# Kernel optimization log

Hardware: AMD Instinct MI355X
Metric: run time of the kernel (lower is better)

The kernel has to match this reference:

```python
import jax, jax.numpy as jnp
import numpy as np

B, S, E, H, ROT, MAXP = 2, 1024, 2048, 16, 64, 2048
HD = E // H
EPS = 1e-12  # torch F.normalize default eps


def _sinusoidal_positions(num_pos, dim):
    # GPT-J create_sinusoidal_positions: concat(sin, cos) along feature dim
    inv_freq = 1.0 / (10000.0 ** (np.arange(0, dim, 2, dtype=np.float32) / dim))
    sinusoid = np.einsum("i,j->ij", np.arange(num_pos, dtype=np.float32), inv_freq)
    return jnp.asarray(np.concatenate([np.sin(sinusoid), np.cos(sinusoid)], axis=-1))


def _rotate_every_two(x):
    x1 = x[..., ::2]
    x2 = x[..., 1::2]
    return jnp.stack((-x2, x1), axis=-1).reshape(x.shape)


def _apply_rotary(t, sin, cos):
    # t: [B,S,H,rot]; sin/cos: [B,S,rot/2] -> repeat_interleave(2) -> [B,S,1,rot]
    sin = jnp.repeat(sin, 2, axis=-1)[:, :, None, :]
    cos = jnp.repeat(cos, 2, axis=-1)[:, :, None, :]
    return t * cos + _rotate_every_two(t) * sin


def setup_inputs() -> dict:
    key = jax.random.key(0)
    ks = jax.random.split(key, 5)
    hidden_states = jax.random.normal(ks[0], (B, S, E), dtype=jnp.float32)
    w_q = jax.random.normal(ks[1], (E, E), dtype=jnp.float32) * 0.02
    w_k = jax.random.normal(ks[2], (E, E), dtype=jnp.float32) * 0.02
    w_v = jax.random.normal(ks[3], (E, E), dtype=jnp.float32) * 0.02
    w_o = jax.random.normal(ks[4], (E, E), dtype=jnp.float32) * 0.02
    norm_const = 0.5 * jnp.ones((1, H, 1, 1), dtype=jnp.float32)
    attention_mask = jnp.zeros((B, 1, 1, S), dtype=jnp.float32)  # 0 = attend (HF additive mask)
    position_ids = jnp.tile(jnp.arange(S, dtype=jnp.int32)[None, :], (B, 1))
    return {"hidden_states": hidden_states, "w_q": w_q, "w_k": w_k, "w_v": w_v,
            "w_o": w_o, "norm_const": norm_const, "attention_mask": attention_mask,
            "position_ids": position_ids}


def reference(hidden_states, w_q, w_k, w_v, w_o, norm_const, attention_mask, position_ids):
    b, s, e = hidden_states.shape
    # projections (nn.Linear, no bias): y = x @ W.T
    q = (hidden_states @ w_q.T).reshape(b, s, H, HD)  # rotary layout [B,S,H,hd]
    k = (hidden_states @ w_k.T).reshape(b, s, H, HD)
    v = (hidden_states @ w_v.T).reshape(b, s, H, HD).transpose(0, 2, 1, 3)  # [B,H,S,hd]

    embed = _sinusoidal_positions(MAXP, ROT)          # [MAXP, ROT]
    sincos = embed[position_ids]                      # [B,S,ROT]
    sin, cos = jnp.split(sincos, 2, axis=-1)          # each [B,S,ROT/2]

    # partial rotary on first ROT dims
    q = jnp.concatenate([_apply_rotary(q[..., :ROT], sin, cos), q[..., ROT:]], axis=-1)
    k = jnp.concatenate([_apply_rotary(k[..., :ROT], sin, cos), k[..., ROT:]], axis=-1)
    q = q.transpose(0, 2, 1, 3)  # [B,H,S,hd]
    k = k.transpose(0, 2, 1, 3)

    causal = jnp.tril(jnp.ones((s, s), dtype=bool))[None, None]   # [1,1,S,S]
    mask0 = (attention_mask == 0)                                  # [B,1,1,S] bool

    # value rescale: per-query count of visible keys ** sigmoid(norm_const), clamped >= 1
    counts = jnp.sum(causal & mask0, axis=-1, keepdims=True).astype(jnp.float32)  # [B,1,S,1]
    denom = jnp.maximum(counts ** jax.nn.sigmoid(norm_const), 1.0)                # [B,H,S,1]
    v = v / denom

    # L2-normalize q/k (torch F.normalize: x / max(||x||, eps))
    q = q / jnp.maximum(jnp.linalg.norm(q, axis=-1, keepdims=True), EPS)
    k = k / jnp.maximum(jnp.linalg.norm(k, axis=-1, keepdims=True), EPS)

    mask_t = jnp.swapaxes(mask0, -1, -2)  # [B,1,S,1]
    q = q * mask_t
    k = k * mask_t
    v = v * mask_t

    attn_weights = jnp.einsum("bhqd,bhkd->bhqk", q, k)     # cosine similarities
    attn_weights = jnp.where(causal, attn_weights, 0.0)
    attn_output = jnp.einsum("bhqk,bhkd->bhqd", attn_weights, v)

    attn_output = attn_output.transpose(0, 2, 1, 3).reshape(b, s, e)
    return attn_output @ w_o.T
```

## Files before the change

kernel.cpp:

```cpp
#include <hip/hip_runtime.h>
#include <math.h>

#define B 2
#define S 1024
#define E 2048
#define H 16
#define HD 128
#define ROT 64
#define EPSN 1e-12f

using half8 = __attribute__((ext_vector_type(8))) _Float16;
using half4 = __attribute__((ext_vector_type(4))) _Float16;
using half2 = __attribute__((ext_vector_type(2))) _Float16;
using f32x4 = __attribute__((ext_vector_type(4))) float;

__device__ __forceinline__ void gl_lds16(const void* g, void* l) {
    __builtin_amdgcn_global_load_lds(
        (const __attribute__((address_space(1))) unsigned int*)g,
        (__attribute__((address_space(3))) unsigned int*)l, 16, 0, 0);
}

#define BARX()  asm volatile("s_barrier" ::: "memory")
#define LGKM0() asm volatile("s_waitcnt lgkmcnt(0)" ::: "memory")
#define VMW(n)  asm volatile("s_waitcnt vmcnt(" #n ")" ::: "memory")

__global__ __launch_bounds__(256) void f2h5(const float* __restrict__ x0,
                                            const float* __restrict__ x1,
                                            const float* __restrict__ x2,
                                            const float* __restrict__ x3,
                                            const float* __restrict__ x4,
                                            _Float16* __restrict__ y0,
                                            _Float16* __restrict__ y1,
                                            _Float16* __restrict__ y2,
                                            _Float16* __restrict__ y3,
                                            _Float16* __restrict__ y4) {
    const float* xs[5] = {x0, x1, x2, x3, x4};
    _Float16*    ys[5] = {y0, y1, y2, y3, y4};
    const int t = blockIdx.y;
    const int i = blockIdx.x * 256 + threadIdx.x;
    float4 v = ((const float4*)xs[t])[i];
    half4 h;
    h[0] = (_Float16)v.x; h[1] = (_Float16)v.y;
    h[2] = (_Float16)v.z; h[3] = (_Float16)v.w;
    ((half4*)ys[t])[i] = h;
}

__global__ __launch_bounds__(512, 2) void gemm_qkv256(
        const _Float16* __restrict__ hs,
        const _Float16* __restrict__ wq,
        const _Float16* __restrict__ wk,
        const _Float16* __restrict__ wv,
        _Float16* __restrict__ qo,
        _Float16* __restrict__ ko,
        _Float16* __restrict__ vo) {
    __shared__ uint4 L[8][1024];

    const int lid = (int)blockIdx.x;
    const int swz = (lid & 7) * 24 + (lid >> 3);
    const int z   = swz >> 6;
    const int gm  = (swz & 63) >> 3;
    const int gn  = swz & 7;
    const _Float16* Wp = (z == 0) ? wq : (z == 1) ? wk : wv;
    _Float16*     Cout = (z == 0) ? qo : (z == 1) ? ko : vo;
    const int mBase = gm << 8;
    const int nBase = gn << 8;

    const int tid   = (int)threadIdx.x;
    const int lane  = tid & 63;
    const int w     = tid >> 6;
    const int l15   = lane & 15;
    const int lq    = lane >> 4;
    const int wm4   = (w >> 2) << 2;
    const int wn2   = (w & 3) << 1;
    const int wbase = tid & 448;

    f32x4 acc[2][2][4][2];
#pragma unroll
    for (int X = 0; X < 2; ++X)
#pragma unroll
        for (int Y = 0; Y < 2; ++Y)
#pragma unroll
            for (int mt = 0; mt < 4; ++mt)
#pragma unroll
                for (int nt = 0; nt < 2; ++nt)
                    acc[X][Y][mt][nt] = (f32x4){0.f, 0.f, 0.f, 0.f};

    half8 af[4][2], wf[2][2];

    auto stage = [&](int slot, const _Float16* src, int rowBase, int hf, int kt) {
#pragma unroll
        for (int j = 0; j < 2; ++j) {
            const int c  = (j << 9) + tid;
            const int rb = c >> 7;
            const int q  = (c >> 4) & 7;
            const int r  = c & 15;
            gl_lds16(&src[(size_t)(rowBase + hf * 128 + rb * 16 + r) * E +
                          kt * 64 + q * 8],
                     &L[slot][(j << 9) + wbase]);
        }
    };
    auto ldsA = [&](int db, int X) {
#pragma unroll
        for (int mt = 0; mt < 4; ++mt)
#pragma unroll
            for (int ks = 0; ks < 2; ++ks)
                af[mt][ks] = *(const half8*)&L[db * 2 + X]
                    [(wm4 + mt) * 128 + (ks * 4 + lq) * 16 + l15];
    };
    auto ldsB = [&](int db, int Y) {
#pragma unroll
        for (int nt = 0; nt < 2; ++nt)
#pragma unroll
            for (int ks = 0; ks < 2; ++ks)
                wf[nt][ks] = *(const half8*)&L[4 + db * 2 + Y]
                    [(wn2 + nt) * 128 + (ks * 4 + lq) * 16 + l15];
    };
    auto mma = [&](int X, int Y) {
        __builtin_amdgcn_s_setprio(1);
#pragma unroll
        for (int mt = 0; mt < 4; ++mt)
#pragma unroll
            for (int nt = 0; nt < 2; ++nt)
#pragma unroll
                for (int ks = 0; ks < 2; ++ks)
                    acc[X][Y][mt][nt] = __builtin_amdgcn_mfma_f32_16x16x32_f16(
                        af[mt][ks], wf[nt][ks], acc[X][Y][mt][nt], 0, 0, 0);
        __builtin_amdgcn_s_setprio(0);
    };

    stage(0, hs, mBase, 0, 0);
    stage(4, Wp, nBase, 0, 0);
    stage(1, hs, mBase, 1, 0);
    stage(5, Wp, nBase, 1, 0);
    stage(2, hs, mBase, 0, 1);
    stage(7, Wp, nBase, 1, 1);
    stage(3, hs, mBase, 1, 1);
    VMW(6);
    BARX();

    for (int j = 0; j < 16; ++j) {
        const int tB  = 2 * j + 1;
        const int tN0 = 2 * j + 2;
        const int tN1 = 2 * j + 3;
        const bool more = (j < 15);

        ldsA(0, 0); ldsB(0, 0);
        stage(6, Wp, nBase, 0, tB);
        BARX(); LGKM0();
        mma(0, 0);
        BARX();

        ldsB(0, 1);
        if (more) stage(0, hs, mBase, 0, tN0);
        BARX(); LGKM0();
        mma(0, 1);
        BARX();

        ldsA(0, 1);
        if (more) stage(5, Wp, nBase, 1, tN0);
        BARX(); LGKM0();
        mma(1, 1);
        BARX();

        ldsB(0, 0);
        if (more) { stage(1, hs, mBase, 1, tN0); VMW(4); }
        else      { VMW(0); }
        BARX(); LGKM0();
        mma(1, 0);
        BARX();

        ldsA(1, 0); ldsB(1, 0);
        if (more) stage(4, Wp, nBase, 0, tN0);
        BARX(); LGKM0();
        mma(0, 0);
        BARX();

        ldsB(1, 1);
        if (more) stage(2, hs, mBase, 0, tN1);
        BARX(); LGKM0();
        mma(0, 1);
        BARX();

        ldsA(1, 1);
        if (more) stage(7, Wp, nBase, 1, tN1);
        BARX(); LGKM0();
        mma(1, 1);
        BARX();

        ldsB(1, 0);
        if (more) stage(3, hs, mBase, 1, tN1);
        VMW(4);
        BARX(); LGKM0();
        mma(1, 0);
        BARX();
    }

#pragma unroll
    for (int X = 0; X < 2; ++X)
#pragma unroll
        for (int Y = 0; Y < 2; ++Y)
#pragma unroll
            for (int mt = 0; mt < 4; ++mt)
#pragma unroll
                for (int nt = 0; nt < 2; ++nt)
#pragma unroll
                    for (int r = 0; r < 4; ++r) {
                        int row = mBase + X * 128 + (w >> 2) * 64 + mt * 16 + lq * 4 + r;
                        int col = nBase + Y * 128 + (w & 3) * 32 + nt * 16 + l15;
                        int b = row >> 10, s = row & (S - 1);
                        int h = col >> 7,  d = col & (HD - 1);
                        Cout[(((size_t)b * H + h) * S + s) * HD + d] =
                            (_Float16)acc[X][Y][mt][nt][r];
                    }
}

__global__ __launch_bounds__(256) void gemm_out(const _Float16* __restrict__ A,
                                                const _Float16* __restrict__ Wp,
                                                float* __restrict__ C) {
    __shared__ uint4 As_l[2][512];
    __shared__ uint4 Ws_l[2][512];
    const int lid = (int)blockIdx.x;
    const int swz = (lid & 7) * 32 + (lid >> 3);
    const int gm  = swz >> 4;
    const int gn  = swz & 15;
    const int tid  = threadIdx.x;
    const int lane = tid & 63;
    const int w    = tid >> 6;
    const int wm   = (w >> 1) * 64;
    const int wn   = (w & 1) * 64;
    const int l15  = lane & 15;
    const int lq   = lane >> 4;
    const int r16  = lane & 15;
    const int kq4  = lane >> 4;
    const int mBase = gm * 128;
    const int nBase = gn * 128;

    f32x4 acc[4][4];
#pragma unroll
    for (int mt = 0; mt < 4; ++mt)
#pragma unroll
        for (int nt = 0; nt < 4; ++nt)
            acc[mt][nt] = (f32x4){0.f, 0.f, 0.f, 0.f};

    auto stage = [&](int bf, int k0) {
#pragma unroll
        for (int i = 0; i < 2; ++i) {
            int rb = w * 2 + i;
            gl_lds16(&A[(size_t)(mBase + rb * 16 + r16) * E + k0 + kq4 * 8],
                     &As_l[bf][rb * 64]);
            gl_lds16(&Wp[(size_t)(nBase + rb * 16 + r16) * E + k0 + kq4 * 8],
                     &Ws_l[bf][rb * 64]);
        }
    };

    stage(0, 0);
    const int nIter = E / 32;
    for (int it = 0; it < nIter; ++it) {
        __syncthreads();
        if (it + 1 < nIter) stage((it + 1) & 1, (it + 1) * 32);

        const int cur = it & 1;
        half8 af[4], wfr[4];
#pragma unroll
        for (int t = 0; t < 4; ++t) {
            int rbA = (wm >> 4) + t;
            int rbW = (wn >> 4) + t;
            af[t]  = *(const half8*)&As_l[cur][rbA * 64 + lq * 16 + l15];
            wfr[t] = *(const half8*)&Ws_l[cur][rbW * 64 + lq * 16 + l15];
        }
#pragma unroll
        for (int mt = 0; mt < 4; ++mt)
#pragma unroll
            for (int nt = 0; nt < 4; ++nt)
                acc[mt][nt] = __builtin_amdgcn_mfma_f32_16x16x32_f16(
                    af[mt], wfr[nt], acc[mt][nt], 0, 0, 0);
    }

#pragma unroll
    for (int mt = 0; mt < 4; ++mt)
#pragma unroll
        for (int nt = 0; nt < 4; ++nt)
#pragma unroll
            for (int r = 0; r < 4; ++r) {
                int row = mBase + wm + mt * 16 + lq * 4 + r;
                int col = nBase + wn + nt * 16 + l15;
                C[(size_t)row * E + col] = acc[mt][nt][r];
            }
}

__global__ __launch_bounds__(256) void rotary_norm(_Float16* __restrict__ qh,
                                                   _Float16* __restrict__ kh,
                                                   const float* __restrict__ am,
                                                   const int* __restrict__ pos) {
    const int wave = threadIdx.x >> 6;
    const int lane = threadIdx.x & 63;
    const int item = blockIdx.x * 4 + wave;
    const int b = item / (H * S);
    const int h = (item / S) % H;
    const int s = item % S;

    const float p = (float)pos[b * S + s];
    float co = 1.f, si = 0.f;
    if (lane < 32) {
        float ang = p * expf(-0.28782313662425574f * (float)lane);
        sincosf(ang, &si, &co);
    }
    const float valid = (am[b * S + s] == 0.f) ? 1.f : 0.f;
    const size_t base = ((size_t)(b * H + h) * S + s) * HD;

    _Float16* bufs[2] = {qh, kh};
#pragma unroll
    for (int a = 0; a < 2; ++a) {
        _Float16* ptr = bufs[a];
        half2 xin = *(const half2*)&ptr[base + 2 * lane];
        float x0 = (float)xin[0], x1 = (float)xin[1];
        float y0, y1;
        if (lane < 32) {
            y0 = x0 * co - x1 * si;
            y1 = x1 * co + x0 * si;
        } else {
            y0 = x0;
            y1 = x1;
        }
        float ss = y0 * y0 + y1 * y1;
#pragma unroll
        for (int off = 32; off > 0; off >>= 1)
            ss += __shfl_xor(ss, off);
        float scale = valid / fmaxf(sqrtf(ss), EPSN);
        half2 xo;
        xo[0] = (_Float16)(y0 * scale);
        xo[1] = (_Float16)(y1 * scale);
        *(half2*)&ptr[base + 2 * lane] = xo;
    }
}

__global__ __launch_bounds__(256) void vprep(const _Float16* __restrict__ v,
                                             const _Float16* __restrict__ k,
                                             _Float16* __restrict__ vt,
                                             _Float16* __restrict__ kt,
                                             const float* __restrict__ am,
                                             const float* __restrict__ nc) {
    __shared__ _Float16 T[HD][72];
    __shared__ float sscale[64];
    const int bh = blockIdx.y;
    const int b = bh >> 4, h = bh & 15;
    const int s0 = blockIdx.x * 64;
    const int tid = threadIdx.x;

    if (tid < 64) {
        const int lane = tid;
        float basec = 0.f;
        for (int j0 = 0; j0 < s0; j0 += 64) {
            float z = (am[b * S + j0 + lane] == 0.f) ? 1.f : 0.f;
#pragma unroll
            for (int off = 32; off > 0; off >>= 1)
                z += __shfl_xor(z, off);
            basec += z;
        }
        float zown = (am[b * S + s0 + lane] == 0.f) ? 1.f : 0.f;
        float sc = zown;
#pragma unroll
        for (int off = 1; off < 64; off <<= 1) {
            float u = __shfl_up(sc, off);
            if (lane >= off) sc += u;
        }
        float cntv = basec + sc;
        float sig = 1.f / (1.f + expf(-nc[h]));
        float denom = fmaxf(powf(cntv, sig), 1.f);
        sscale[lane] = zown / denom;
    }
    __syncthreads();

#pragma unroll
    for (int j = 0; j < 4; ++j) {
        int f = tid + j * 256;
        int s = f >> 4, c8 = f & 15;
        half8 x = *(const half8*)&v[((size_t)bh * S + s0 + s) * HD + c8 * 8];
        float sc = sscale[s];
#pragma unroll
        for (int i = 0; i < 8; ++i)
            T[c8 * 8 + i][s] = (_Float16)((float)x[i] * sc);
    }
    __syncthreads();
#pragma unroll
    for (int j = 0; j < 4; ++j) {
        int f = tid + j * 256;
        int d = f >> 3, c8 = f & 7;
        *(uint4*)&vt[((size_t)bh * HD + d) * S + s0 + c8 * 8] =
            *(const uint4*)&T[d][c8 * 8];
    }

    __syncthreads();
#pragma unroll
    for (int j = 0; j < 4; ++j) {
        int f = tid + j * 256;
        int s = f >> 4, c8 = f & 15;
        half8 x = *(const half8*)&k[((size_t)bh * S + s0 + s) * HD + c8 * 8];
#pragma unroll
        for (int i = 0; i < 8; ++i)
            T[c8 * 8 + i][s] = x[i];
    }
    __syncthreads();
#pragma unroll
    for (int j = 0; j < 4; ++j) {
        int f = tid + j * 256;
        int d = f >> 3, c8 = f & 7;
        *(uint4*)&kt[((size_t)bh * HD + d) * S + s0 + c8 * 8] =
            *(const uint4*)&T[d][c8 * 8];
    }
}

__global__ __launch_bounds__(256) void kvouter(const _Float16* __restrict__ kt,
                                               const _Float16* __restrict__ vt,
                                               _Float16* __restrict__ ut) {
    __shared__ __align__(16) _Float16 SB[2 * 128 * 72];
    _Float16 (*Kt_s)[72] = (_Float16(*)[72])SB;
    _Float16 (*Vt_s)[72] = (_Float16(*)[72])(SB + 128 * 72);
    const int c  = blockIdx.x;
    const int bh = blockIdx.y;
    const int tid = threadIdx.x;
    const int lane = tid & 63, w = tid >> 6;
    const int l15 = lane & 15, lq = lane >> 4;
    const size_t ds_b = (size_t)bh * HD * S + (size_t)c * 64;

    uint4 pk[4], pv[4];
#pragma unroll
    for (int j = 0; j < 4; ++j) {
        int f = tid + j * 256;
        int d = f >> 3, c8 = f & 7;
        pk[j] = *(const uint4*)&kt[ds_b + (size_t)d * S + c8 * 8];
        pv[j] = *(const uint4*)&vt[ds_b + (size_t)d * S + c8 * 8];
    }
#pragma unroll
    for (int j = 0; j < 4; ++j) {
        int f = tid + j * 256;
        int d = f >> 3, c8 = f & 7;
        *(uint4*)&Kt_s[d][c8 * 8] = pk[j];
        *(uint4*)&Vt_s[d][c8 * 8] = pv[j];
    }
    __syncthreads();

    f32x4 acc[2][8];
#pragma unroll
    for (int mt = 0; mt < 2; ++mt)
#pragma unroll
        for (int nt = 0; nt < 8; ++nt)
            acc[mt][nt] = (f32x4){0.f, 0.f, 0.f, 0.f};

#pragma unroll
    for (int ks = 0; ks < 2; ++ks) {
        half8 af[2], wf[8];
#pragma unroll
        for (int mt = 0; mt < 2; ++mt)
            af[mt] = *(const half8*)&Kt_s[(w * 2 + mt) * 16 + l15][ks * 32 + lq * 8];
#pragma unroll
        for (int nt = 0; nt < 8; ++nt)
            wf[nt] = *(const half8*)&Vt_s[nt * 16 + l15][ks * 32 + lq * 8];
#pragma unroll
        for (int mt = 0; mt < 2; ++mt)
#pragma unroll
            for (int nt = 0; nt < 8; ++nt)
                acc[mt][nt] = __builtin_amdgcn_mfma_f32_16x16x32_f16(
                    af[mt], wf[nt], acc[mt][nt], 0, 0, 0);
    }
    __syncthreads();

    _Float16* Mb = SB;
#pragma unroll
    for (int mt = 0; mt < 2; ++mt)
#pragma unroll
        for (int nt = 0; nt < 8; ++nt)
#pragma unroll
            for (int r = 0; r < 4; ++r) {
                int dk = (w * 2 + mt) * 16 + lq * 4 + r;
                int flat = nt * 2048 + (dk >> 5) * 512 +
                           (l15 + ((dk >> 3) & 3) * 16) * 8 + (dk & 7);
                Mb[flat] = (_Float16)acc[mt][nt][r];
            }
    __syncthreads();

    const size_t ub = ((size_t)bh * 16 + c) << 14;
#pragma unroll
    for (int j = 0; j < 8; ++j) {
        int f = tid + j * 256;
        *(uint4*)&ut[ub + (size_t)f * 8] = *(const uint4*)&Mb[f * 8];
    }
}

__global__ __launch_bounds__(256) void prefix16(_Float16* __restrict__ u) {
    const int sl = blockIdx.x & 7;
    const int bh = blockIdx.x >> 3;
    const size_t base = (size_t)bh * 16 * 16384 + sl * 2048 + threadIdx.x * 8;
    float acc[8] = {0.f, 0.f, 0.f, 0.f, 0.f, 0.f, 0.f, 0.f};
    half8 nxt = *(const half8*)&u[base];
#pragma unroll
    for (int c = 0; c < 16; ++c) {
        half8 cur = nxt;
        if (c < 15) nxt = *(const half8*)&u[base + (size_t)(c + 1) * 16384];
        half8 outv;
#pragma unroll
        for (int i = 0; i < 8; ++i) outv[i] = (_Float16)acc[i];
        *(half8*)&u[base + (size_t)c * 16384] = outv;
#pragma unroll
        for (int i = 0; i < 8; ++i) acc[i] += (float)cur[i];
    }
}

__global__ __launch_bounds__(256) void attn_local(const _Float16* __restrict__ qh,
                                                  const _Float16* __restrict__ kh,
                                                  const _Float16* __restrict__ vt,
                                                  const _Float16* __restrict__ mt,
                                                  _Float16* __restrict__ o) {
    __shared__ _Float16 Ks[64][136];
    __shared__ _Float16 Vs[HD][72];
    __shared__ _Float16 Ps[64][72];
    __shared__ uint4 Ms[2048];

    const int qt = blockIdx.x;
    const int bh = blockIdx.y;
    const int b = bh >> 4, h = bh & 15;
    const int tid = threadIdx.x;
    const int lane = tid & 63;
    const int w = tid >> 6;
    const int l15 = lane & 15;
    const int lq = lane >> 4;
    const int qBase = qt * 64;
    const size_t sd_base = (size_t)bh * S * HD;

    half8 qf[4];
#pragma unroll
    for (int ks = 0; ks < 4; ++ks)
        qf[ks] = *(const half8*)&qh[sd_base + (size_t)(qBase + w * 16 + l15) * HD +
                                    ks * 32 + lq * 8];

    const _Float16* mtc = mt + (((size_t)bh * 16 + qt) << 14);
#pragma unroll
    for (int rr = 0; rr < 8; ++rr)
        gl_lds16(&mtc[(size_t)((rr * 4 + w) * 64 + lane) * 8],
                 &Ms[(rr * 4 + w) * 64]);

    uint4 pk[4], pv[4];
#pragma unroll
    for (int j = 0; j < 4; ++j) {
        int f = tid + j * 256;
        int rK = f >> 4, c8K = f & 15;
        int rV = f >> 3, c8V = f & 7;
        pk[j] = *(const uint4*)&kh[sd_base + (size_t)(qBase + rK) * HD + c8K * 8];
        pv[j] = *(const uint4*)&vt[sd_base + (size_t)rV * S + qBase + c8V * 8];
    }
#pragma unroll
    for (int j = 0; j < 4; ++j) {
        int f = tid + j * 256;
        int rK = f >> 4, c8K = f & 15;
        int rV = f >> 3, c8V = f & 7;
        *(uint4*)&Ks[rK][c8K * 8] = pk[j];
        *(uint4*)&Vs[rV][c8V * 8] = pv[j];
    }
    __syncthreads();

    f32x4 sacc[4];
#pragma unroll
    for (int nt = 0; nt < 4; ++nt)
        sacc[nt] = (f32x4){0.f, 0.f, 0.f, 0.f};
#pragma unroll
    for (int nt = 0; nt < 4; ++nt)
#pragma unroll
        for (int ks = 0; ks < 4; ++ks) {
            half8 kf = *(const half8*)&Ks[nt * 16 + l15][ks * 32 + lq * 8];
            sacc[nt] = __builtin_amdgcn_mfma_f32_16x16x32_f16(qf[ks], kf,
                                                              sacc[nt], 0, 0, 0);
        }

#pragma unroll
    for (int nt = 0; nt < 4; ++nt)
#pragma unroll
        for (int r = 0; r < 4; ++r) {
            int ql = w * 16 + lq * 4 + r;
            int kl = nt * 16 + l15;
            float sv = (kl <= ql) ? sacc[nt][r] : 0.f;
            Ps[ql][kl] = (_Float16)sv;
        }

    f32x4 oacc[8];
#pragma unroll
    for (int dt = 0; dt < 8; ++dt)
        oacc[dt] = (f32x4){0.f, 0.f, 0.f, 0.f};
#pragma unroll
    for (int dt = 0; dt < 8; ++dt)
#pragma unroll
        for (int km = 0; km < 4; ++km) {
            half8 mf = *(const half8*)&Ms[(dt * 4 + km) * 64 + lane];
            oacc[dt] = __builtin_amdgcn_mfma_f32_16x16x32_f16(qf[km], mf,
                                                              oacc[dt], 0, 0, 0);
        }
    __syncthreads();

    half8 pf[2];
    pf[0] = *(const half8*)&Ps[w * 16 + l15][lq * 8];
    pf[1] = *(const half8*)&Ps[w * 16 + l15][32 + lq * 8];
#pragma unroll
    for (int dt = 0; dt < 8; ++dt)
#pragma unroll
        for (int ks = 0; ks < 2; ++ks) {
            half8 vf = *(const half8*)&Vs[dt * 16 + l15][ks * 32 + lq * 8];
            oacc[dt] = __builtin_amdgcn_mfma_f32_16x16x32_f16(pf[ks], vf,
                                                              oacc[dt], 0, 0, 0);
        }

#pragma unroll
    for (int dt = 0; dt < 8; ++dt)
#pragma unroll
        for (int r = 0; r < 4; ++r)
            Ks[w * 16 + lq * 4 + r][dt * 16 + l15] = (_Float16)oacc[dt][r];
    __syncthreads();
#pragma unroll
    for (int j = 0; j < 4; ++j) {
        int f = tid + j * 256;
        int ql = f >> 4, c8 = f & 15;
        *(uint4*)&o[(size_t)(b * S + qBase + ql) * E + h * HD + c8 * 8] =
            *(const uint4*)&Ks[ql][c8 * 8];
    }
}

extern "C" void kernel_launch(void* const* d_in, const int* in_sizes, int n_in,
                              void* d_out, int out_size, void* d_ws, size_t ws_size,
                              hipStream_t stream) {
    (void)in_sizes; (void)n_in; (void)out_size; (void)ws_size;
    const float* hs = (const float*)d_in[0];
    const float* wq = (const float*)d_in[1];
    const float* wk = (const float*)d_in[2];
    const float* wv = (const float*)d_in[3];
    const float* wo = (const float*)d_in[4];
    const float* nc = (const float*)d_in[5];
    const float* am = (const float*)d_in[6];
    const int*  pos = (const int*)d_in[7];
    float* out = (float*)d_out;

    const size_t act = (size_t)B * S * E;
    _Float16* hsb = (_Float16*)d_ws;
    _Float16* wqb = hsb + act;
    _Float16* wkb = wqb + act;
    _Float16* wvb = wkb + act;
    _Float16* wob = wvb + act;
    _Float16* qhh = wob + act;
    _Float16* khh = qhh + act;
    _Float16* vhh = khh + act;
    _Float16* vtt = vhh + act;
    _Float16* abb = vtt + act;
    _Float16* ktt = hsb;
    _Float16* utm = wqb;

    f2h5<<<dim3((int)(act / 4 / 256), 5), 256, 0, stream>>>(
        hs, wq, wk, wv, wo, hsb, wqb, wkb, wvb, wob);

    gemm_qkv256<<<192, 512, 0, stream>>>(hsb, wqb, wkb, wvb, qhh, khh, vhh);

    rotary_norm<<<(B * H * S) / 4, 256, 0, stream>>>(qhh, khh, am, pos);
    vprep<<<dim3(S / 64, B * H), 256, 0, stream>>>(vhh, khh, vtt, ktt, am, nc);

    kvouter<<<dim3(16, B * H), 256, 0, stream>>>(ktt, vtt, utm);
    prefix16<<<B * H * 8, 256, 0, stream>>>(utm);
    attn_local<<<dim3(16, B * H), 256, 0, stream>>>(qhh, khh, vtt, utm, abb);

    gemm_out<<<256, 256, 0, stream>>>(abb, wob, out);
}
```

Before: 301.4 us.

## Fuse rotary, normalization, V scaling and K/V transposes into QKV GEMM epilogue

Moves the rotary embedding, L2 normalization, mask application, V count-based rescale and the K/V transposes into the epilogue of the QKV projection GEMM. The epilogue stages the output tile through LDS with a swizzled index, and a small prefix-count kernel precomputes the visible-key counts. This removes two separate kernels and their global round trips of Q/K/V. The GEMM main loop is also re-pipelined with register double buffering of the A/B fragments and sched barriers in place of the explicit lgkmcnt waits, which trades higher register pressure for overlap of LDS reads with MFMA.

```diff
diff --git a/kernel.cpp b/kernel.cpp
--- a/kernel.cpp
+++ b/kernel.cpp
@@ -20,9 +20,13 @@
         (__attribute__((address_space(3))) unsigned int*)l, 16, 0, 0);
 }
 
-#define BARX()  asm volatile("s_barrier" ::: "memory")
-#define LGKM0() asm volatile("s_waitcnt lgkmcnt(0)" ::: "memory")
-#define VMW(n)  asm volatile("s_waitcnt vmcnt(" #n ")" ::: "memory")
+#define BARX()   asm volatile("s_barrier" ::: "memory")
+#define VMW(n)   asm volatile("s_waitcnt vmcnt(" #n ")" ::: "memory")
+#define SCHEDB() __builtin_amdgcn_sched_barrier(0)
+
+__device__ __forceinline__ int ctIdx(int row, int col) {
+    return row * 256 + (col & 3) + ((((col >> 2) ^ ((row >> 3) & 15)) & 63) << 2);
+}
 
 __global__ __launch_bounds__(256) void f2h5(const float* __restrict__ x0,
                                             const float* __restrict__ x1,
@@ -45,6 +49,21 @@
     ((half4*)ys[t])[i] = h;
 }
 
+__global__ __launch_bounds__(1024) void countprep(const float* __restrict__ am,
+                                                  float* __restrict__ cnt) {
+    __shared__ float sc[1024];
+    const int b = blockIdx.x, t = threadIdx.x;
+    sc[t] = (am[b * S + t] == 0.f) ? 1.f : 0.f;
+    __syncthreads();
+    for (int off = 1; off < 1024; off <<= 1) {
+        float u = (t >= off) ? sc[t - off] : 0.f;
+        __syncthreads();
+        sc[t] += u;
+        __syncthreads();
+    }
+    cnt[b * S + t] = sc[t];
+}
+
 __global__ __launch_bounds__(512, 2) void gemm_qkv256(
         const _Float16* __restrict__ hs,
         const _Float16* __restrict__ wq,
@@ -52,8 +71,14 @@
         const _Float16* __restrict__ wv,
         _Float16* __restrict__ qo,
         _Float16* __restrict__ ko,
-        _Float16* __restrict__ vo) {
+        _Float16* __restrict__ kto,
+        _Float16* __restrict__ vto,
+        const float* __restrict__ am,
+        const int*  __restrict__ pos,
+        const float* __restrict__ nc,
+        const float* __restrict__ cnt) {
     __shared__ uint4 L[8][1024];
+    __shared__ float sclA[256], sclB[256];
 
     const int lid = (int)blockIdx.x;
     const int swz = (lid & 7) * 24 + (lid >> 3);
@@ -61,7 +86,6 @@
     const int gm  = (swz & 63) >> 3;
     const int gn  = swz & 7;
     const _Float16* Wp = (z == 0) ? wq : (z == 1) ? wk : wv;
-    _Float16*     Cout = (z == 0) ? qo : (z == 1) ? ko : vo;
     const int mBase = gm << 8;
     const int nBase = gn << 8;
 
@@ -74,6 +98,24 @@
     const int wn2   = (w & 3) << 1;
     const int wbase = tid & 448;
 
+    const int bb  = mBase >> 10;
+    const int sB0 = mBase & (S - 1);
+    const int h0  = gn * 2;
+
+    if (tid < 256) {
+        const int sgx = sB0 + tid;
+        float valid = (am[bb * S + sgx] == 0.f) ? 1.f : 0.f;
+        if (z == 2) {
+            float c  = cnt[bb * S + sgx];
+            float g0 = 1.f / (1.f + expf(-nc[h0]));
+            float g1 = 1.f / (1.f + expf(-nc[h0 + 1]));
+            sclA[tid] = valid / fmaxf(powf(c, g0), 1.f);
+            sclB[tid] = valid / fmaxf(powf(c, g1), 1.f);
+        } else {
+            sclA[tid] = valid;
+        }
+    }
+
     f32x4 acc[2][2][4][2];
 #pragma unroll
     for (int X = 0; X < 2; ++X)
@@ -85,7 +127,7 @@
                 for (int nt = 0; nt < 2; ++nt)
                     acc[X][Y][mt][nt] = (f32x4){0.f, 0.f, 0.f, 0.f};
 
-    half8 af[4][2], wf[2][2];
+    half8 afA[4][2], afB[4][2], wfA[2][2], wfB[2][2];
 
     auto stage = [&](int slot, const _Float16* src, int rowBase, int hf, int kt) {
 #pragma unroll
@@ -99,34 +141,33 @@
                      &L[slot][(j << 9) + wbase]);
         }
     };
-    auto ldsA = [&](int db, int X) {
+    auto ldsA = [&](half8 (&dst)[4][2], int slot) {
 #pragma unroll
         for (int mt = 0; mt < 4; ++mt)
 #pragma unroll
             for (int ks = 0; ks < 2; ++ks)
-                af[mt][ks] = *(const half8*)&L[db * 2 + X]
+                dst[mt][ks] = *(const half8*)&L[slot]
                     [(wm4 + mt) * 128 + (ks * 4 + lq) * 16 + l15];
     };
-    auto ldsB = [&](int db, int Y) {
+    auto ldsB = [&](half8 (&dst)[2][2], int slot) {
 #pragma unroll
         for (int nt = 0; nt < 2; ++nt)
 #pragma unroll
             for (int ks = 0; ks < 2; ++ks)
-                wf[nt][ks] = *(const half8*)&L[4 + db * 2 + Y]
+                dst[nt][ks] = *(const half8*)&L[slot]
                     [(wn2 + nt) * 128 + (ks * 4 + lq) * 16 + l15];
     };
-    auto mma = [&](int X, int Y) {
-        __builtin_amdgcn_s_setprio(1);
-#pragma unroll
-        for (int mt = 0; mt < 4; ++mt)
-#pragma unroll
-            for (int nt = 0; nt < 2; ++nt)
-#pragma unroll
-                for (int ks = 0; ks < 2; ++ks)
-                    acc[X][Y][mt][nt] = __builtin_amdgcn_mfma_f32_16x16x32_f16(
-                        af[mt][ks], wf[nt][ks], acc[X][Y][mt][nt], 0, 0, 0);
-        __builtin_amdgcn_s_setprio(0);
-    };
+
+#define MMAQ(X, Y, Af, Bf)                                                     \
+    do {                                                                       \
+        __builtin_amdgcn_s_setprio(1);                                         \
+        _Pragma("unroll") for (int mt = 0; mt < 4; ++mt)                       \
+            _Pragma("unroll") for (int nt = 0; nt < 2; ++nt)                   \
+                _Pragma("unroll") for (int ks = 0; ks < 2; ++ks)               \
+                    acc[X][Y][mt][nt] = __builtin_amdgcn_mfma_f32_16x16x32_f16(\
+                        Af[mt][ks], Bf[nt][ks], acc[X][Y][mt][nt], 0, 0, 0);   \
+        __builtin_amdgcn_s_setprio(0);                                         \
+    } while (0)
 
     stage(0, hs, mBase, 0, 0);
     stage(4, Wp, nBase, 0, 0);
@@ -137,6 +178,8 @@
     stage(3, hs, mBase, 1, 1);
     VMW(6);
     BARX();
+    ldsA(afA, 0);
+    ldsB(wfA, 4);
 
     for (int j = 0; j < 16; ++j) {
         const int tB  = 2 * j + 1;
@@ -144,57 +187,59 @@
         const int tN1 = 2 * j + 3;
         const bool more = (j < 15);
 
-        ldsA(0, 0); ldsB(0, 0);
+        BARX();
+        ldsB(wfB, 5);
         stage(6, Wp, nBase, 0, tB);
-        BARX(); LGKM0();
-        mma(0, 0);
-        BARX();
-
-        ldsB(0, 1);
+        SCHEDB();
+        MMAQ(0, 0, afA, wfA);
+
+        BARX();
+        ldsA(afB, 1);
         if (more) stage(0, hs, mBase, 0, tN0);
-        BARX(); LGKM0();
-        mma(0, 1);
-        BARX();
-
-        ldsA(0, 1);
+        SCHEDB();
+        MMAQ(0, 1, afA, wfB);
+
+        BARX();
         if (more) stage(5, Wp, nBase, 1, tN0);
-        BARX(); LGKM0();
-        mma(1, 1);
-        BARX();
-
-        ldsB(0, 0);
-        if (more) { stage(1, hs, mBase, 1, tN0); VMW(4); }
-        else      { VMW(0); }
-        BARX(); LGKM0();
-        mma(1, 0);
-        BARX();
-
-        ldsA(1, 0); ldsB(1, 0);
+        SCHEDB();
+        MMAQ(1, 1, afB, wfB);
+
+        if (more) { VMW(4); } else { VMW(0); }
+        BARX();
+        ldsA(afA, 2);
+        ldsB(wfB, 6);
+        if (more) stage(1, hs, mBase, 1, tN0);
+        SCHEDB();
+        MMAQ(1, 0, afB, wfA);
+
+        BARX();
+        ldsB(wfA, 7);
         if (more) stage(4, Wp, nBase, 0, tN0);
-        BARX(); LGKM0();
-        mma(0, 0);
-        BARX();
-
-        ldsB(1, 1);
+        SCHEDB();
+        MMAQ(0, 0, afA, wfB);
+
+        BARX();
+        ldsA(afB, 3);
         if (more) stage(2, hs, mBase, 0, tN1);
-        BARX(); LGKM0();
-        mma(0, 1);
-        BARX();
-
-        ldsA(1, 1);
+        SCHEDB();
+        MMAQ(0, 1, afA, wfA);
+
+        BARX();
         if (more) stage(7, Wp, nBase, 1, tN1);
-        BARX(); LGKM0();
-        mma(1, 1);
-        BARX();
-
-        ldsB(1, 0);
+        SCHEDB();
+        MMAQ(1, 1, afB, wfA);
+
+        VMW(4);
+        BARX();
+        ldsA(afA, 0);
+        ldsB(wfA, 4);
         if (more) stage(3, hs, mBase, 1, tN1);
-        VMW(4);
-        BARX(); LGKM0();
-        mma(1, 0);
-        BARX();
-    }
-
+        SCHEDB();
+        MMAQ(1, 0, afB, wfB);
+    }
+
+    BARX();
+    _Float16* CtH = (_Float16*)&L[0][0];
 #pragma unroll
     for (int X = 0; X < 2; ++X)
 #pragma unroll
@@ -205,13 +250,65 @@
                 for (int nt = 0; nt < 2; ++nt)
 #pragma unroll
                     for (int r = 0; r < 4; ++r) {
-                        int row = mBase + X * 128 + (w >> 2) * 64 + mt * 16 + lq * 4 + r;
-                        int col = nBase + Y * 128 + (w & 3) * 32 + nt * 16 + l15;
-                        int b = row >> 10, s = row & (S - 1);
-                        int h = col >> 7,  d = col & (HD - 1);
-                        Cout[(((size_t)b * H + h) * S + s) * HD + d] =
-                            (_Float16)acc[X][Y][mt][nt][r];
+                        int row = X * 128 + (w >> 2) * 64 + mt * 16 + lq * 4 + r;
+                        int col = Y * 128 + (w & 3) * 32 + nt * 16 + l15;
+                        float v = acc[X][Y][mt][nt][r];
+                        if (z == 2) v *= (Y ? sclB[row] : sclA[row]);
+                        CtH[ctIdx(row, col)] = (_Float16)v;
                     }
+    __syncthreads();
+
+    if (z < 2) {
+        _Float16* rowOut = (z == 0) ? qo : ko;
+        const int hh = lane >> 5;
+        const int il = lane & 31;
+        for (int rr = 0; rr < 32; ++rr) {
+            int row = w * 32 + rr;
+            int sg  = sB0 + row;
+            float p = (float)pos[bb * S + sg];
+            half4 x = *(const half4*)&CtH[ctIdx(row, hh * 128 + il * 4)];
+            float v0 = x[0], v1 = x[1], v2 = x[2], v3 = x[3];
+            if (il < 16) {
+                float a0 = p * expf(-0.28782313662425574f * (float)(2 * il));
+                float a1 = p * expf(-0.28782313662425574f * (float)(2 * il + 1));
+                float s0, c0, s1, c1;
+                sincosf(a0, &s0, &c0);
+                sincosf(a1, &s1, &c1);
+                float t0 = v0 * c0 - v1 * s0, t1 = v1 * c0 + v0 * s0;
+                float t2 = v2 * c1 - v3 * s1, t3 = v3 * c1 + v2 * s1;
+                v0 = t0; v1 = t1; v2 = t2; v3 = t3;
+            }
+            float ss = v0 * v0 + v1 * v1 + v2 * v2 + v3 * v3;
+            ss += __shfl_xor(ss, 1);  ss += __shfl_xor(ss, 2);
+            ss += __shfl_xor(ss, 4);  ss += __shfl_xor(ss, 8);
+            ss += __shfl_xor(ss, 16);
+            float scl = sclA[row] / fmaxf(sqrtf(ss), EPSN);
+            half4 y;
+            y[0] = (_Float16)(v0 * scl); y[1] = (_Float16)(v1 * scl);
+            y[2] = (_Float16)(v2 * scl); y[3] = (_Float16)(v3 * scl);
+            *(half4*)&rowOut[(((size_t)bb * H + h0 + hh) * S + sg) * HD +
+                             il * 4] = y;
+            if (z == 1)
+                *(half4*)&CtH[ctIdx(row, hh * 128 + il * 4)] = y;
+        }
+    }
+    if (z >= 1) {
+        if (z == 1) __syncthreads();
+        _Float16* To = (z == 1) ? kto : vto;
+#pragma unroll
+        for (int i = 0; i < 16; ++i) {
+            int cch = tid + i * 512;
+            int dr  = cch >> 5;
+            int sc  = cch & 31;
+            half8 hv;
+#pragma unroll
+            for (int jj = 0; jj < 8; ++jj)
+                hv[jj] = CtH[ctIdx(sc * 8 + jj, dr)];
+            *(half8*)&To[(((size_t)bb * H + h0 + (dr >> 7)) * HD + (dr & 127)) * S +
+                         sB0 + sc * 8] = hv;
+        }
+    }
+#undef MMAQ
 }
 
 __global__ __launch_bounds__(256) void gemm_out(const _Float16* __restrict__ A,
@@ -288,128 +385,6 @@
             }
 }
 
-__global__ __launch_bounds__(256) void rotary_norm(_Float16* __restrict__ qh,
-                                                   _Float16* __restrict__ kh,
-                                                   const float* __restrict__ am,
-                                                   const int* __restrict__ pos) {
-    const int wave = threadIdx.x >> 6;
-    const int lane = threadIdx.x & 63;
-    const int item = blockIdx.x * 4 + wave;
-    const int b = item / (H * S);
-    const int h = (item / S) % H;
-    const int s = item % S;
-
-    const float p = (float)pos[b * S + s];
-    float co = 1.f, si = 0.f;
-    if (lane < 32) {
-        float ang = p * expf(-0.28782313662425574f * (float)lane);
-        sincosf(ang, &si, &co);
-    }
-    const float valid = (am[b * S + s] == 0.f) ? 1.f : 0.f;
-    const size_t base = ((size_t)(b * H + h) * S + s) * HD;
-
-    _Float16* bufs[2] = {qh, kh};
-#pragma unroll
-    for (int a = 0; a < 2; ++a) {
-        _Float16* ptr = bufs[a];
-        half2 xin = *(const half2*)&ptr[base + 2 * lane];
-        float x0 = (float)xin[0], x1 = (float)xin[1];
-        float y0, y1;
-        if (lane < 32) {
-            y0 = x0 * co - x1 * si;
-            y1 = x1 * co + x0 * si;
-        } else {
-            y0 = x0;
-            y1 = x1;
-        }
-        float ss = y0 * y0 + y1 * y1;
-#pragma unroll
-        for (int off = 32; off > 0; off >>= 1)
-            ss += __shfl_xor(ss, off);
-        float scale = valid / fmaxf(sqrtf(ss), EPSN);
-        half2 xo;
-        xo[0] = (_Float16)(y0 * scale);
-        xo[1] = (_Float16)(y1 * scale);
-        *(half2*)&ptr[base + 2 * lane] = xo;
-    }
-}
-
-__global__ __launch_bounds__(256) void vprep(const _Float16* __restrict__ v,
-                                             const _Float16* __restrict__ k,
-                                             _Float16* __restrict__ vt,
-                                             _Float16* __restrict__ kt,
-                                             const float* __restrict__ am,
-                                             const float* __restrict__ nc) {
-    __shared__ _Float16 T[HD][72];
-    __shared__ float sscale[64];
-    const int bh = blockIdx.y;
-    const int b = bh >> 4, h = bh & 15;
-    const int s0 = blockIdx.x * 64;
-    const int tid = threadIdx.x;
-
-    if (tid < 64) {
-        const int lane = tid;
-        float basec = 0.f;
-        for (int j0 = 0; j0 < s0; j0 += 64) {
-            float z = (am[b * S + j0 + lane] == 0.f) ? 1.f : 0.f;
-#pragma unroll
-            for (int off = 32; off > 0; off >>= 1)
-                z += __shfl_xor(z, off);
-            basec += z;
-        }
-        float zown = (am[b * S + s0 + lane] == 0.f) ? 1.f : 0.f;
-        float sc = zown;
-#pragma unroll
-        for (int off = 1; off < 64; off <<= 1) {
-            float u = __shfl_up(sc, off);
-            if (lane >= off) sc += u;
-        }
-        float cntv = basec + sc;
-        float sig = 1.f / (1.f + expf(-nc[h]));
-        float denom = fmaxf(powf(cntv, sig), 1.f);
-        sscale[lane] = zown / denom;
-    }
-    __syncthreads();
-
-#pragma unroll
-    for (int j = 0; j < 4; ++j) {
-        int f = tid + j * 256;
-        int s = f >> 4, c8 = f & 15;
-        half8 x = *(const half8*)&v[((size_t)bh * S + s0 + s) * HD + c8 * 8];
-        float sc = sscale[s];
-#pragma unroll
-        for (int i = 0; i < 8; ++i)
-            T[c8 * 8 + i][s] = (_Float16)((float)x[i] * sc);
-    }
-    __syncthreads();
-#pragma unroll
-    for (int j = 0; j < 4; ++j) {
-        int f = tid + j * 256;
-        int d = f >> 3, c8 = f & 7;
-        *(uint4*)&vt[((size_t)bh * HD + d) * S + s0 + c8 * 8] =
-            *(const uint4*)&T[d][c8 * 8];
-    }
-
-    __syncthreads();
-#pragma unroll
-    for (int j = 0; j < 4; ++j) {
-        int f = tid + j * 256;
-        int s = f >> 4, c8 = f & 15;
-        half8 x = *(const half8*)&k[((size_t)bh * S + s0 + s) * HD + c8 * 8];
-#pragma unroll
-        for (int i = 0; i < 8; ++i)
-            T[c8 * 8 + i][s] = x[i];
-    }
-    __syncthreads();
-#pragma unroll
-    for (int j = 0; j < 4; ++j) {
-        int f = tid + j * 256;
-        int d = f >> 3, c8 = f & 7;
-        *(uint4*)&kt[((size_t)bh * HD + d) * S + s0 + c8 * 8] =
-            *(const uint4*)&T[d][c8 * 8];
-    }
-}
-
 __global__ __launch_bounds__(256) void kvouter(const _Float16* __restrict__ kt,
                                                const _Float16* __restrict__ vt,
                                                _Float16* __restrict__ ut) {
@@ -644,19 +619,19 @@
     _Float16* wob = wvb + act;
     _Float16* qhh = wob + act;
     _Float16* khh = qhh + act;
-    _Float16* vhh = khh + act;
-    _Float16* vtt = vhh + act;
+    _Float16* ktt = khh + act;
+    _Float16* vtt = ktt + act;
     _Float16* abb = vtt + act;
-    _Float16* ktt = hsb;
     _Float16* utm = wqb;
+    float*    cnt = (float*)abb;
 
     f2h5<<<dim3((int)(act / 4 / 256), 5), 256, 0, stream>>>(
         hs, wq, wk, wv, wo, hsb, wqb, wkb, wvb, wob);
 
-    gemm_qkv256<<<192, 512, 0, stream>>>(hsb, wqb, wkb, wvb, qhh, khh, vhh);
-
-    rotary_norm<<<(B * H * S) / 4, 256, 0, stream>>>(qhh, khh, am, pos);
-    vprep<<<dim3(S / 64, B * H), 256, 0, stream>>>(vhh, khh, vtt, ktt, am, nc);
+    countprep<<<B, 1024, 0, stream>>>(am, cnt);
+
+    gemm_qkv256<<<192, 512, 0, stream>>>(hsb, wqb, wkb, wvb,
+                                         qhh, khh, ktt, vtt, am, pos, nc, cnt);
 
     kvouter<<<dim3(16, B * H), 256, 0, stream>>>(ktt, vtt, utm);
     prefix16<<<B * H * 8, 256, 0, stream>>>(utm);
```

Result: slower. 357.9 us (+18.8%).
